# Optimization experiments

Measured on AMD Instinct MI355X. Metric: run time of the kernel, lower is better.

Reference implementation:

```python
import jax, jax.numpy as jnp
import numpy as np

BS, S, D, H = 2, 2048, 1024, 16
DH = D // H  # 64


def setup_inputs() -> dict:
    key = jax.random.key(0)
    k1, k2, k3 = jax.random.split(key, 3)
    x = jax.random.normal(k1, (BS, S, D), dtype=jnp.float32)
    w_qkv = jax.random.normal(k2, (D, H, 3 * DH), dtype=jnp.float32) * (D ** -0.5)
    b_qkv = jnp.zeros((H, 3 * DH), dtype=jnp.float32)
    w_out = jax.random.normal(k3, (H, DH, D), dtype=jnp.float32) * (D ** -0.5)
    b_out = jnp.zeros((D,), dtype=jnp.float32)
    return {"x": x, "w_qkv": w_qkv, "b_qkv": b_qkv, "w_out": w_out, "b_out": b_out}


def reference(x, w_qkv, b_qkv, w_out, b_out):
    dtype = x.dtype
    # QKV projection: DenseGeneral(features=(H, 3*DH)) -> [B, S, H, 3*DH]
    qkv = jnp.einsum("bsd,dhf->bshf", x, w_qkv) + b_qkv
    q, k, v = jnp.split(qkv, 3, axis=-1)  # each [B, S, H, DH]

    scale = DH ** -0.5
    q = (q * scale).astype(jnp.float32)
    k = k.astype(jnp.float32)
    # Full causal attention with fp32 scores (as in original)
    weights = jnp.einsum("bqhd,bkhd->bhqk", q, k)  # [B, H, S, S]
    causal = jnp.tril(jnp.ones((S, S), dtype=bool))[None, None, :, :]
    weights = jnp.where(causal, weights, jnp.finfo(jnp.float32).min)
    weights = jax.nn.softmax(weights, axis=-1).astype(dtype)
    attn = jnp.einsum("bhqk,bkhd->bqhd", weights, v).astype(dtype)

    # Output projection: DenseGeneral(D, axis=(-2, -1))
    out = jnp.einsum("bqhd,hdo->bqo", attn, w_out) + b_out
    return out
```

## Files before the change

kernel.cpp:

```cpp
#include <hip/hip_runtime.h>
#include <hip/hip_bf16.h>
#include <stdint.h>

#define NBS 2
#define SEQ 2048
#define DMODEL 1024
#define NH 16
#define DHEAD 64
#define MROWS (NBS*SEQ)
#define NQKV (NH*3*DHEAD)

typedef __bf16 bf16;
typedef __bf16 bf16x8 __attribute__((ext_vector_type(8)));
typedef float f32x4 __attribute__((ext_vector_type(4)));
typedef float f32x16 __attribute__((ext_vector_type(16)));
typedef unsigned int u32x2 __attribute__((ext_vector_type(2)));

#define LOG2E 1.44269504088896f
#define QSCALE (0.125f * LOG2E)
#define KSTR 72

static __device__ __forceinline__ void gload_lds16(const bf16* g, bf16* l) {
    __builtin_amdgcn_global_load_lds(
        (const __attribute__((address_space(1))) uint32_t*)g,
        (__attribute__((address_space(3))) uint32_t*)l, 16, 0, 0);
}

static __device__ __forceinline__ bf16x8 ld_b8(const bf16* p) {
    return __builtin_bit_cast(bf16x8, *(const uint4*)p);
}

static __device__ __forceinline__ uint32_t pk_bf16(float lo, float hi) {
    unsigned short l = __builtin_bit_cast(unsigned short, (bf16)lo);
    unsigned short h = __builtin_bit_cast(unsigned short, (bf16)hi);
    return ((uint32_t)h << 16) | (uint32_t)l;
}

static __device__ __forceinline__ u32x2 lane_swap32(uint32_t a, uint32_t b, int lane) {
#if __has_builtin(__builtin_amdgcn_permlane32_swap)
    return __builtin_amdgcn_permlane32_swap(a, b, false, false);
#else
    uint32_t sa = __shfl_xor(a, 32), sb = __shfl_xor(b, 32);
    u32x2 r;
    r.x = (lane >= 32) ? sb : a;
    r.y = (lane >= 32) ? b : sa;
    return r;
#endif
}

__global__ __launch_bounds__(256) void k_prep(
        const float* __restrict__ x, const float* __restrict__ w_qkv,
        const float* __restrict__ w_out,
        bf16* __restrict__ xb, bf16* __restrict__ wqkT, bf16* __restrict__ woT) {
    __shared__ float t[32][33];
    int bid = blockIdx.x, tid = threadIdx.x;
    if (bid < 4096) {
        int i = bid * 256 + tid;
        float4 v = ((const float4*)x)[i];
        ushort4 o;
        o.x = __builtin_bit_cast(unsigned short, (bf16)v.x);
        o.y = __builtin_bit_cast(unsigned short, (bf16)v.y);
        o.z = __builtin_bit_cast(unsigned short, (bf16)v.z);
        o.w = __builtin_bit_cast(unsigned short, (bf16)v.w);
        ((ushort4*)xb)[i] = o;
    } else if (bid < 7168) {
        int lb = bid - 4096;
        int bx = lb % 96, by = lb / 96;
        int tx = tid & 31, ty = tid >> 5;
        int r0 = by * 32, c0 = bx * 32;
#pragma unroll
        for (int i = 0; i < 4; i++)
            t[ty + i*8][tx] = w_qkv[(size_t)(r0 + ty + i*8) * NQKV + (c0 + tx)];
        __syncthreads();
#pragma unroll
        for (int i = 0; i < 4; i++) {
            int c = c0 + ty + i*8;
            int h = c / 192, f = c % 192;
            int cperm = ((f >> 6) << 10) + (h << 6) + (f & 63);
            wqkT[(size_t)cperm * DMODEL + (r0 + tx)] = (bf16)t[tx][ty + i*8];
        }
    } else {
        int lb = bid - 7168;
        int bx = lb & 31, by = lb >> 5;
        int tx = tid & 31, ty = tid >> 5;
        int r0 = by * 32, c0 = bx * 32;
#pragma unroll
        for (int i = 0; i < 4; i++)
            t[ty + i*8][tx] = w_out[(size_t)(r0 + ty + i*8) * DMODEL + (c0 + tx)];
        __syncthreads();
#pragma unroll
        for (int i = 0; i < 4; i++)
            woT[(size_t)(c0 + ty + i*8) * DMODEL + (r0 + tx)] = (bf16)t[tx][ty + i*8];
    }
}

#define G1_NT 16

__global__ __launch_bounds__(512, 2) void k_gemm_qkv(
        const bf16* __restrict__ A, const bf16* __restrict__ Bt,
        const float* __restrict__ bias,
        bf16* __restrict__ Q, bf16* __restrict__ Kp, bf16* __restrict__ Vt) {
    __shared__ __align__(16) bf16 As[2][256*64];
    __shared__ __align__(16) bf16 Bs[2][192*64];
    int tid = threadIdx.x;
    int wid = tid >> 6, lane = tid & 63;
    int wr = wid >> 2, wc = wid & 3;
    int g = lane >> 4, r = lane & 15;

    int lid = blockIdx.y * 16 + blockIdx.x;
    int swz = (lid & 7) * 32 + (lid >> 3);
    int tile_n = (swz % 16) * 192, tile_m = (swz / 16) * 256;

    f32x4 acc[8][3];
#pragma unroll
    for (int m = 0; m < 8; m++)
#pragma unroll
        for (int n = 0; n < 3; n++)
            acc[m][n] = (f32x4){0.f, 0.f, 0.f, 0.f};

    int srowA[4], schkA[4], srowB[3], schkB[3];
#pragma unroll
    for (int j2 = 0; j2 < 4; j2++) {
        int idx = tid + j2 * 512;
        srowA[j2] = idx >> 3;
        schkA[j2] = ((idx & 7) ^ (srowA[j2] & 7)) * 8;
    }
#pragma unroll
    for (int j2 = 0; j2 < 3; j2++) {
        int idx = tid + j2 * 512;
        srowB[j2] = idx >> 3;
        schkB[j2] = ((idx & 7) ^ (srowB[j2] & 7)) * 8;
    }

#define G1_STAGE(buf, k0)                                                          \
    {                                                                              \
        _Pragma("unroll")                                                          \
        for (int j2 = 0; j2 < 4; j2++)                                             \
            gload_lds16(A + (size_t)(tile_m + srowA[j2]) * DMODEL + (k0) + schkA[j2], \
                        As[buf] + (tid + j2*512) * 8);                             \
        _Pragma("unroll")                                                          \
        for (int j2 = 0; j2 < 3; j2++)                                             \
            gload_lds16(Bt + (size_t)(tile_n + srowB[j2]) * DMODEL + (k0) + schkB[j2], \
                        Bs[buf] + (tid + j2*512) * 8);                             \
    }

    G1_STAGE(0, 0);

    int r7 = r & 7;
    for (int t = 0; t < G1_NT; t++) {
        int cur = t & 1;
        if (t + 1 < G1_NT) {
            G1_STAGE(cur ^ 1, (t + 1) * 64);
            asm volatile("s_waitcnt vmcnt(7)" ::: "memory");
        } else {
            asm volatile("s_waitcnt vmcnt(0)" ::: "memory");
        }
        __builtin_amdgcn_s_barrier();
        __builtin_amdgcn_sched_barrier(0);

        const bf16* pa = As[cur];
        const bf16* pb = Bs[cur];
#pragma unroll
        for (int kk = 0; kk < 2; kk++) {
            int rchk = ((kk*4 + g) ^ r7) * 8;
            bf16x8 bfr[3];
#pragma unroll
            for (int n = 0; n < 3; n++)
                bfr[n] = ld_b8(pb + (wc*48 + n*16 + r) * 64 + rchk);
#pragma unroll
            for (int m = 0; m < 8; m++) {
                bf16x8 af = ld_b8(pa + (wr*128 + m*16 + r) * 64 + rchk);
#pragma unroll
                for (int n = 0; n < 3; n++)
                    acc[m][n] = __builtin_amdgcn_mfma_f32_16x16x32_bf16(af, bfr[n], acc[m][n], 0, 0, 0);
            }
        }
        asm volatile("s_waitcnt lgkmcnt(0)" ::: "memory");
        __builtin_amdgcn_s_barrier();
    }

#pragma unroll
    for (int m = 0; m < 8; m++) {
#pragma unroll
        for (int n = 0; n < 3; n++) {
            int col = tile_n + wc*48 + n*16 + r;
            int kind = col >> 10;
            int h = (col >> 6) & 15;
            int d = col & 63;
            float bv = bias[h*192 + (kind << 6) + d];
            if (kind == 2) {
                int row0 = tile_m + wr*128 + m*16 + g*4;
                int b = row0 >> 11, s0 = row0 & 2047;
                ushort4 vv;
                vv.x = __builtin_bit_cast(unsigned short, (bf16)(acc[m][n][0] + bv));
                vv.y = __builtin_bit_cast(unsigned short, (bf16)(acc[m][n][1] + bv));
                vv.z = __builtin_bit_cast(unsigned short, (bf16)(acc[m][n][2] + bv));
                vv.w = __builtin_bit_cast(unsigned short, (bf16)(acc[m][n][3] + bv));
                *(ushort4*)&Vt[(((size_t)(b*NH + h)) * DHEAD + d) * SEQ + s0] = vv;
            } else {
#pragma unroll
                for (int j = 0; j < 4; j++) {
                    int row = tile_m + wr*128 + m*16 + g*4 + j;
                    int b = row >> 11, s = row & 2047;
                    float v = acc[m][n][j] + bv;
                    size_t addr = (((size_t)(b*NH + h)) * SEQ + s) * DHEAD + d;
                    if (kind == 0) Q[addr]  = (bf16)(v * QSCALE);
                    else           Kp[addr] = (bf16)v;
                }
            }
        }
    }
#undef G1_STAGE
}

__global__ __launch_bounds__(256) void k_gemm_out(
        const bf16* __restrict__ A, const bf16* __restrict__ Bt,
        const float* __restrict__ bias, float* __restrict__ out) {
    __shared__ __align__(16) bf16 As[2][64*32];
    __shared__ __align__(16) bf16 Bs[2][128*32];
    int tid = threadIdx.x;
    int wave = tid >> 6, lane = tid & 63;
    int g = lane >> 4, r = lane & 15;
    int srow = lane >> 2, schunk = (lane & 3) * 8;
    int tile_m = blockIdx.y * 64, tile_n = blockIdx.x * 128;

    f32x4 acc[4][2];
#pragma unroll
    for (int m = 0; m < 4; m++)
#pragma unroll
        for (int n = 0; n < 2; n++)
            acc[m][n] = (f32x4){0.f, 0.f, 0.f, 0.f};

#define GO_STAGE(buf, k0)                                                                 \
    {                                                                                     \
        gload_lds16(A  + (size_t)(tile_m + wave*16 + srow) * DMODEL + (k0) + schunk,      \
                    As[buf] + wave*512);                                                  \
        gload_lds16(Bt + (size_t)(tile_n + wave*16 + srow) * DMODEL + (k0) + schunk,      \
                    Bs[buf] + wave*512);                                                  \
        gload_lds16(Bt + (size_t)(tile_n + 64 + wave*16 + srow) * DMODEL + (k0) + schunk, \
                    Bs[buf] + 2048 + wave*512);                                           \
    }

    GO_STAGE(0, 0);

    for (int t = 0; t < 32; t++) {
        int cur = t & 1;
        if (t + 1 < 32) {
            GO_STAGE(cur ^ 1, (t + 1) * 32);
            asm volatile("s_waitcnt vmcnt(3)" ::: "memory");
        } else {
            asm volatile("s_waitcnt vmcnt(0)" ::: "memory");
        }
        __builtin_amdgcn_s_barrier();
        __builtin_amdgcn_sched_barrier(0);

        bf16x8 af[4], bfr[2];
#pragma unroll
        for (int m = 0; m < 4; m++) af[m]  = *(const bf16x8*)(As[cur] + (m*16 + r)*32 + g*8);
#pragma unroll
        for (int n = 0; n < 2; n++) bfr[n] = *(const bf16x8*)(Bs[cur] + (wave*32 + n*16 + r)*32 + g*8);
#pragma unroll
        for (int m = 0; m < 4; m++)
#pragma unroll
            for (int n = 0; n < 2; n++)
                acc[m][n] = __builtin_amdgcn_mfma_f32_16x16x32_bf16(af[m], bfr[n], acc[m][n], 0, 0, 0);
        asm volatile("s_waitcnt lgkmcnt(0)" ::: "memory");
        __builtin_amdgcn_s_barrier();
    }
#undef GO_STAGE

#pragma unroll
    for (int m = 0; m < 4; m++) {
#pragma unroll
        for (int n = 0; n < 2; n++) {
            int col = tile_n + wave*32 + n*16 + r;
            float bv = bias[col];
#pragma unroll
            for (int j = 0; j < 4; j++) {
                int row = tile_m + m*16 + g*4 + j;
                out[(size_t)row * DMODEL + col] = acc[m][n][j] + bv;
            }
        }
    }
}

#define QBLK 128
#define KVB 64

static __device__ __forceinline__ void attn_tile_body(
        const bf16* Ks, const bf16* VsT,
        const bf16x8 qa2[4], const bf16x8& ones,
        f32x16 o32[2], f32x16& acc_l,
        int kv0, int qb, int qrow, int l31, int hi, int lane) {
    const f32x16 z16 = {0,0,0,0,0,0,0,0,0,0,0,0,0,0,0,0};
    f32x16 st[2];
    st[0] = z16; st[1] = z16;
    __builtin_amdgcn_s_setprio(1);
#pragma unroll
    for (int c = 0; c < 4; c++) {
        bf16x8 kf0 = ld_b8(Ks + l31*KSTR        + c*16 + hi*8);
        bf16x8 kf1 = ld_b8(Ks + (32 + l31)*KSTR + c*16 + hi*8);
        st[0] = __builtin_amdgcn_mfma_f32_32x32x16_bf16(kf0, qa2[c], st[0], 0, 0, 0);
        st[1] = __builtin_amdgcn_mfma_f32_32x32x16_bf16(kf1, qa2[c], st[1], 0, 0, 0);
    }
    __builtin_amdgcn_s_setprio(0);

    bf16x8 vf[2][4];
#pragma unroll
    for (int dblk = 0; dblk < 2; dblk++)
#pragma unroll
        for (int c = 0; c < 4; c++)
            vf[dblk][c] = ld_b8(VsT + (dblk*32 + l31)*KSTR + c*16 + hi*8);

    bool needm = (kv0 + KVB - 1) > qb;
#pragma unroll
    for (int rb = 0; rb < 2; rb++) {
#pragma unroll
        for (int reg = 0; reg < 16; reg++) {
            float e = __builtin_amdgcn_exp2f(st[rb][reg]);
            if (needm) {
                int kv = kv0 + rb*32 + (reg & 3) + 8*(reg >> 2) + 4*hi;
                if (kv > qrow) e = 0.f;
            }
            st[rb][reg] = e;
        }
    }

    bf16x8 pa[4];
#pragma unroll
    for (int c = 0; c < 4; c++) {
        const f32x16& pp = st[c >> 1];
        const int base = (c & 1) * 8;
        uint32_t a0 = pk_bf16(pp[base+0], pp[base+1]);
        uint32_t a1 = pk_bf16(pp[base+2], pp[base+3]);
        uint32_t b0 = pk_bf16(pp[base+4], pp[base+5]);
        uint32_t b1 = pk_bf16(pp[base+6], pp[base+7]);
        u32x2 s0 = lane_swap32(a0, b0, lane);
        u32x2 s1 = lane_swap32(a1, b1, lane);
        uint4 fr = {s0.x, s1.x, s0.y, s1.y};
        pa[c] = __builtin_bit_cast(bf16x8, fr);
    }

    __builtin_amdgcn_s_setprio(1);
#pragma unroll
    for (int c = 0; c < 4; c++) {
        o32[0] = __builtin_amdgcn_mfma_f32_32x32x16_bf16(pa[c], vf[0][c], o32[0], 0, 0, 0);
        o32[1] = __builtin_amdgcn_mfma_f32_32x32x16_bf16(pa[c], vf[1][c], o32[1], 0, 0, 0);
        acc_l  = __builtin_amdgcn_mfma_f32_32x32x16_bf16(pa[c], ones, acc_l, 0, 0, 0);
    }
    __builtin_amdgcn_s_setprio(0);
}

__device__ const int8_t JQC[32]  = {10,10, 4, 0, 15,15, 3, 1,  9, 9, 7, 2, 13,14, 7, 5,
                                    14,14,11, 5, 15, 8,11, 6,  8,12,12, 6, 13,13,11,12};
__device__ const int8_t JT0[32]  = { 0,11, 0, 0,  0,11, 0, 0,  0,10, 0, 0,  0, 0, 8, 0,
                                    10,20, 0, 6, 22, 0, 8, 0,  9, 0, 9, 7, 10,19,16,18};
__device__ const int8_t JT1[32]  = {11,22,10, 2, 11,22, 8, 4, 10,20, 8, 6, 10,10,16, 6,
                                    20,30, 8,12, 32, 9,16, 7, 18, 9,18,14, 19,28,24,26};
__device__ const int8_t JSEG[32] = { 0, 1, 0, 0,  0, 1, 0, 0,  0, 1, 0, 0,  0, 0, 1, 0,
                                     1, 2, 0, 1,  2, 0, 1, 0,  1, 0, 1, 1,  1, 2, 2, 2};

__global__ __launch_bounds__(256) void k_attn_split(
        const bf16* __restrict__ Q, const bf16* __restrict__ K,
        const bf16* __restrict__ Vt,
        bf16* __restrict__ Op0, bf16* __restrict__ Op1, bf16* __restrict__ Op2,
        float* __restrict__ Lp0, float* __restrict__ Lp1, float* __restrict__ Lp2) {
    int scu = blockIdx.x;
    int bh = scu >> 3, slot = scu & 7;
    int j = slot * 4 + blockIdx.y;
    int qc  = JQC[j];
    int t0  = JT0[j];
    int t1  = JT1[j];
    int seg = JSEG[j];
    int q0 = qc * QBLK;
    int tid = threadIdx.x, wave = tid >> 6, lane = tid & 63;
    int l31 = lane & 31, hi = lane >> 5;

    __shared__ __align__(16) bf16 Ks[2][KVB*KSTR];
    __shared__ __align__(16) bf16 VsT[2][KVB*KSTR];

    const bf16* Kg = K  + (size_t)bh * SEQ * DHEAD;
    const bf16* Vg = Vt + (size_t)bh * DHEAD * SEQ;

    int qb = q0 + wave * 32;
    int qrow = qb + l31;

    const bf16* qrow_p = Q + ((size_t)bh * SEQ + qrow) * DHEAD;
    bf16x8 qa2[4];
#pragma unroll
    for (int c = 0; c < 4; c++) qa2[c] = ld_b8(qrow_p + c*16 + hi*8);

    bf16x8 ones;
#pragma unroll
    for (int c = 0; c < 8; c++) ones[c] = (bf16)1.0f;

    const f32x16 z16 = {0,0,0,0,0,0,0,0,0,0,0,0,0,0,0,0};
    f32x16 o32[2], acc_l;
    o32[0] = z16; o32[1] = z16; acc_l = z16;

    int qmax_wave = qb + 31;

    int srow = tid >> 3, sc8 = (tid & 7) * 8;
    int wK0 = srow*KSTR + sc8;
    int wK1 = (srow+32)*KSTR + sc8;

    bf16x8 kreg[2], vreg[2];
    {
        int kvs = t0 * KVB;
        kreg[0] = ld_b8(Kg + (size_t)(kvs + srow)      * DHEAD + sc8);
        kreg[1] = ld_b8(Kg + (size_t)(kvs + srow + 32) * DHEAD + sc8);
        vreg[0] = ld_b8(Vg + (size_t)srow      * SEQ + kvs + sc8);
        vreg[1] = ld_b8(Vg + (size_t)(srow+32) * SEQ + kvs + sc8);
    }

    int cur = 0;
    for (int t = t0; t < t1; t++) {
        int kv0 = t * KVB;
        *(uint4*)&Ks[cur][wK0]  = __builtin_bit_cast(uint4, kreg[0]);
        *(uint4*)&Ks[cur][wK1]  = __builtin_bit_cast(uint4, kreg[1]);
        *(uint4*)&VsT[cur][wK0] = __builtin_bit_cast(uint4, vreg[0]);
        *(uint4*)&VsT[cur][wK1] = __builtin_bit_cast(uint4, vreg[1]);
        __syncthreads();

        if (t + 1 < t1) {
            int kv1 = kv0 + KVB;
            kreg[0] = ld_b8(Kg + (size_t)(kv1 + srow)      * DHEAD + sc8);
            kreg[1] = ld_b8(Kg + (size_t)(kv1 + srow + 32) * DHEAD + sc8);
            vreg[0] = ld_b8(Vg + (size_t)srow      * SEQ + kv1 + sc8);
            vreg[1] = ld_b8(Vg + (size_t)(srow+32) * SEQ + kv1 + sc8);
        }

        if (kv0 <= qmax_wave)
            attn_tile_body(Ks[cur], VsT[cur], qa2, ones, o32, acc_l,
                           kv0, qb, qrow, l31, hi, lane);
        cur ^= 1;
    }

    bf16* Op; float* Lp; size_t obase; int lbase;
    if (seg == 0)      { Op = Op0; Lp = Lp0; obase = ((size_t)bh*2048 + q0) * 64;          lbase = bh*2048 + q0; }
    else if (seg == 1) { Op = Op1; Lp = Lp1; obase = ((size_t)bh*1408 + (qc-5)*128) * 64;  lbase = bh*1408 + (qc-5)*128; }
    else               { Op = Op2; Lp = Lp2; obase = ((size_t)bh*640  + (qc-11)*128) * 64; lbase = bh*640  + (qc-11)*128; }

    if (l31 == 0) {
#pragma unroll
        for (int reg = 0; reg < 16; reg++) {
            int qr = (reg & 3) + 8*(reg >> 2) + 4*hi;
            Lp[lbase + wave*32 + qr] = acc_l[reg];
        }
    }

#pragma unroll
    for (int reg = 0; reg < 16; reg++) {
        int qr = (reg & 3) + 8*(reg >> 2) + 4*hi;
        size_t base = obase + (size_t)(wave*32 + qr) * 64 + l31;
        Op[base]      = (bf16)o32[0][reg];
        Op[base + 32] = (bf16)o32[1][reg];
    }
}

__global__ __launch_bounds__(256) void k_merge(
        const bf16* __restrict__ Op0, const bf16* __restrict__ Op1,
        const bf16* __restrict__ Op2,
        const float* __restrict__ Lp0, const float* __restrict__ Lp1,
        const float* __restrict__ Lp2,
        bf16* __restrict__ Oa) {
    int g = blockIdx.x * 256 + threadIdx.x;
    int dseg = g & 7;
    int s = (g >> 3) & 2047;
    int bh = g >> 14;
    int qc = s >> 7;
    int sl = s & 127;

    size_t r0 = ((size_t)bh * 2048 + s) * 64 + dseg*8;
    bf16x8 p0 = ld_b8(Op0 + r0);
    float l = Lp0[bh*2048 + s];
    float acc[8];
#pragma unroll
    for (int i = 0; i < 8; i++) acc[i] = (float)p0[i];

    if (qc >= 5) {
        size_t r1 = ((size_t)bh * 1408 + (qc-5)*128 + sl) * 64 + dseg*8;
        bf16x8 p1 = ld_b8(Op1 + r1);
        l += Lp1[bh*1408 + (qc-5)*128 + sl];
#pragma unroll
        for (int i = 0; i < 8; i++) acc[i] += (float)p1[i];
        if (qc >= 11) {
            size_t r2 = ((size_t)bh * 640 + (qc-11)*128 + sl) * 64 + dseg*8;
            bf16x8 p2 = ld_b8(Op2 + r2);
            l += Lp2[bh*640 + (qc-11)*128 + sl];
#pragma unroll
            for (int i = 0; i < 8; i++) acc[i] += (float)p2[i];
        }
    }

    float inv = 1.0f / l;
    bf16x8 r;
#pragma unroll
    for (int i = 0; i < 8; i++) r[i] = (bf16)(acc[i] * inv);
    int b = bh >> 4, h = bh & 15;
    *(uint4*)&Oa[(((size_t)b * SEQ + s) * NH + h) * DHEAD + dseg*8] =
        __builtin_bit_cast(uint4, r);
}

__global__ __launch_bounds__(256) void k_attn(
        const bf16* __restrict__ Q, const bf16* __restrict__ K,
        const bf16* __restrict__ Vt, bf16* __restrict__ O) {
    int bh = blockIdx.y;
    int qc = (bh >= 16) ? (15 - (int)blockIdx.x) : (int)blockIdx.x;
    int q0 = qc * QBLK;
    int tid = threadIdx.x, wave = tid >> 6, lane = tid & 63;
    int l31 = lane & 31, hi = lane >> 5;

    __shared__ __align__(16) bf16 Ks[2][KVB*KSTR];
    __shared__ __align__(16) bf16 VsT[2][KVB*KSTR];

    const bf16* Kg = K  + (size_t)bh * SEQ * DHEAD;
    const bf16* Vg = Vt + (size_t)bh * DHEAD * SEQ;

    int qb = q0 + wave * 32;
    int qrow = qb + l31;

    const bf16* qrow_p = Q + ((size_t)bh * SEQ + qrow) * DHEAD;
    bf16x8 qa2[4];
#pragma unroll
    for (int c = 0; c < 4; c++) qa2[c] = ld_b8(qrow_p + c*16 + hi*8);

    bf16x8 ones;
#pragma unroll
    for (int c = 0; c < 8; c++) ones[c] = (bf16)1.0f;

    const f32x16 z16 = {0,0,0,0,0,0,0,0,0,0,0,0,0,0,0,0};
    f32x16 o32[2], acc_l;
    o32[0] = z16; o32[1] = z16; acc_l = z16;

    int nt = 2*qc + 2;
    int qmax_wave = qb + 31;

    int srow = tid >> 3, sc8 = (tid & 7) * 8;
    int wK0 = srow*KSTR + sc8;
    int wK1 = (srow+32)*KSTR + sc8;

    bf16x8 kreg[2], vreg[2];
    kreg[0] = ld_b8(Kg + (size_t)srow      * DHEAD + sc8);
    kreg[1] = ld_b8(Kg + (size_t)(srow+32) * DHEAD + sc8);
    vreg[0] = ld_b8(Vg + (size_t)srow      * SEQ + sc8);
    vreg[1] = ld_b8(Vg + (size_t)(srow+32) * SEQ + sc8);

    int cur = 0;
    for (int t = 0; t < nt; t++) {
        int kv0 = t * KVB;
        *(uint4*)&Ks[cur][wK0]  = __builtin_bit_cast(uint4, kreg[0]);
        *(uint4*)&Ks[cur][wK1]  = __builtin_bit_cast(uint4, kreg[1]);
        *(uint4*)&VsT[cur][wK0] = __builtin_bit_cast(uint4, vreg[0]);
        *(uint4*)&VsT[cur][wK1] = __builtin_bit_cast(uint4, vreg[1]);
        __syncthreads();

        if (t + 1 < nt) {
            int kv1 = kv0 + KVB;
            kreg[0] = ld_b8(Kg + (size_t)(kv1 + srow)      * DHEAD + sc8);
            kreg[1] = ld_b8(Kg + (size_t)(kv1 + srow + 32) * DHEAD + sc8);
            vreg[0] = ld_b8(Vg + (size_t)srow      * SEQ + kv1 + sc8);
            vreg[1] = ld_b8(Vg + (size_t)(srow+32) * SEQ + kv1 + sc8);
        }

        if (kv0 <= qmax_wave)
            attn_tile_body(Ks[cur], VsT[cur], qa2, ones, o32, acc_l,
                           kv0, qb, qrow, l31, hi, lane);
        cur ^= 1;
    }

    int b = bh >> 4, h = bh & 15;
#pragma unroll
    for (int reg = 0; reg < 16; reg++) {
        int qr = (reg & 3) + 8*(reg >> 2) + 4*hi;
        int srow2 = q0 + wave*32 + qr;
        float linv = 1.0f / acc_l[reg];
        size_t base = (((size_t)b * SEQ + srow2) * NH + h) * DHEAD + l31;
        O[base]      = (bf16)(o32[0][reg] * linv);
        O[base + 32] = (bf16)(o32[1][reg] * linv);
    }
}


extern "C" void kernel_launch(void* const* d_in, const int* in_sizes, int n_in,
                              void* d_out, int out_size, void* d_ws, size_t ws_size,
                              hipStream_t stream) {
    const float* x     = (const float*)d_in[0];
    const float* w_qkv = (const float*)d_in[1];
    const float* b_qkv = (const float*)d_in[2];
    const float* w_out = (const float*)d_in[3];
    const float* b_out = (const float*)d_in[4];
    float* out = (float*)d_out;

    char* ws = (char*)d_ws;
    bf16* xb   = (bf16*)(ws);
    bf16* wqkT = (bf16*)(ws + 8388608);
    bf16* woT  = (bf16*)(ws + 14680064);
    bf16* qb   = (bf16*)(ws + 16777216);
    bf16* kb   = (bf16*)(ws + 25165824);
    bf16* vb   = (bf16*)(ws + 33554432);
    bf16* Op0  = (bf16*)(ws + 41943040);
    bf16* Op1  = (bf16*)(ws + 50331648);
    bf16* Op2  = (bf16*)(ws + 56098816);
    float* Lp0 = (float*)(ws + 8388608);
    float* Lp1 = (float*)(ws + 8388608 + 262144);
    float* Lp2 = (float*)(ws + 8388608 + 524288);
    const size_t WS_NEED = 58720256;
    bf16* attn = xb;

    k_prep<<<8192, 256, 0, stream>>>(x, w_qkv, w_out, xb, wqkT, woT);

    k_gemm_qkv<<<dim3(16, 16), 512, 0, stream>>>(xb, wqkT, b_qkv, qb, kb, vb);

    if (ws_size >= WS_NEED) {
        k_attn_split<<<dim3(256, 4), 256, 0, stream>>>(qb, kb, vb,
                                                       Op0, Op1, Op2, Lp0, Lp1, Lp2);
        k_merge<<<(NBS*NH*SEQ*DHEAD/8)/256, 256, 0, stream>>>(Op0, Op1, Op2,
                                                              Lp0, Lp1, Lp2, attn);
    } else {
        k_attn<<<dim3(SEQ/QBLK, NBS*NH), 256, 0, stream>>>(qb, kb, vb, attn);
    }

    k_gemm_out<<<dim3(DMODEL/128, MROWS/64), 256, 0, stream>>>(attn, woT, b_out, out);
}
```

Measured before the change: 115.3 us.

## Fuse split-attention merge into output projection GEMM A-tile loading

Removes the separate merge kernel and instead combines the three partial attention outputs and their normalizers while loading A tiles in the output GEMM. This drops one kernel launch plus the write and reread of the merged attention tensor. In exchange, each of the 8 column-tile blocks redoes the merge for its rows, and every load reads all three partials unconditionally, masked by multipliers. Those reads use clamped indices, so they fetch real but unused data, adding global traffic to the GEMM's critical path.

```diff
diff --git a/kernel.cpp b/kernel.cpp
--- a/kernel.cpp
+++ b/kernel.cpp
@@ -213,6 +213,117 @@
 #undef G1_STAGE
 }
 
+__global__ __launch_bounds__(256) void k_gemm_out_f(
+        const bf16* __restrict__ Op0, const bf16* __restrict__ Op1,
+        const bf16* __restrict__ Op2,
+        const float* __restrict__ Lp0, const float* __restrict__ Lp1,
+        const float* __restrict__ Lp2,
+        const bf16* __restrict__ Bt, const float* __restrict__ bias,
+        float* __restrict__ out) {
+    __shared__ __align__(16) bf16 As[2][64*32];
+    __shared__ __align__(16) bf16 Bs[2][128*32];
+    int tid = threadIdx.x;
+    int wave = tid >> 6, lane = tid & 63;
+    int g = lane >> 4, r = lane & 15;
+    int srow = lane >> 2, schunk = (lane & 3) * 8;
+    int tile_m = blockIdx.y * 64, tile_n = blockIdx.x * 128;
+
+    int row = tile_m + wave*16 + srow;
+    int b = row >> 11, s = row & 2047;
+    int qc = s >> 7, sl = s & 127;
+    int qc5  = (qc >= 5)  ? qc - 5  : 0;
+    int qc11 = (qc >= 11) ? qc - 11 : 0;
+    float u1 = (qc >= 5)  ? 1.f : 0.f;
+    float u2 = (qc >= 11) ? 1.f : 0.f;
+    int i1 = qc5*128 + sl, i2 = qc11*128 + sl;
+
+    f32x4 acc[4][2];
+#pragma unroll
+    for (int m = 0; m < 4; m++)
+#pragma unroll
+        for (int n = 0; n < 2; n++)
+            acc[m][n] = (f32x4){0.f, 0.f, 0.f, 0.f};
+
+#define A_LOAD(t, p0v, p1v, p2v, l0v, l1v, l2v)                                   \
+    {                                                                             \
+        int h_ = (t) >> 1, d0_ = ((t) & 1) * 32 + schunk;                         \
+        int bh_ = b*16 + h_;                                                      \
+        p0v = *(const uint4*)&Op0[((size_t)bh_*2048 + s)*64 + d0_];               \
+        p1v = *(const uint4*)&Op1[((size_t)bh_*1408 + i1)*64 + d0_];              \
+        p2v = *(const uint4*)&Op2[((size_t)bh_*640  + i2)*64 + d0_];              \
+        l0v = Lp0[bh_*2048 + s]; l1v = Lp1[bh_*1408 + i1]; l2v = Lp2[bh_*640 + i2]; \
+    }
+
+#define A_MERGE(buf, p0v, p1v, p2v, l0v, l1v, l2v)                                \
+    {                                                                             \
+        bf16x8 q0_ = __builtin_bit_cast(bf16x8, p0v);                             \
+        bf16x8 q1_ = __builtin_bit_cast(bf16x8, p1v);                             \
+        bf16x8 q2_ = __builtin_bit_cast(bf16x8, p2v);                             \
+        float inv_ = 1.0f / (l0v + u1*l1v + u2*l2v);                              \
+        bf16x8 mg_;                                                               \
+        _Pragma("unroll")                                                         \
+        for (int i_ = 0; i_ < 8; i_++)                                            \
+            mg_[i_] = (bf16)((((float)q0_[i_]) + u1*(float)q1_[i_]                \
+                              + u2*(float)q2_[i_]) * inv_);                       \
+        *(uint4*)&As[buf][(wave*16 + srow)*32 + schunk] =                         \
+            __builtin_bit_cast(uint4, mg_);                                       \
+    }
+
+#define B_STAGE(buf, k0)                                                                  \
+    {                                                                                     \
+        gload_lds16(Bt + (size_t)(tile_n + wave*16 + srow) * DMODEL + (k0) + schunk,      \
+                    Bs[buf] + wave*512);                                                  \
+        gload_lds16(Bt + (size_t)(tile_n + 64 + wave*16 + srow) * DMODEL + (k0) + schunk, \
+                    Bs[buf] + 2048 + wave*512);                                           \
+    }
+
+    uint4 pa0, pa1, pa2;
+    float la0, la1, la2;
+
+    A_LOAD(0, pa0, pa1, pa2, la0, la1, la2);
+    B_STAGE(0, 0);
+    A_MERGE(0, pa0, pa1, pa2, la0, la1, la2);
+    __syncthreads();
+
+    for (int t = 0; t < 32; t++) {
+        int cur = t & 1;
+        if (t + 1 < 32) {
+            A_LOAD(t + 1, pa0, pa1, pa2, la0, la1, la2);
+            B_STAGE(cur ^ 1, (t + 1) * 32);
+        }
+        bf16x8 af[4], bfr[2];
+#pragma unroll
+        for (int m = 0; m < 4; m++) af[m]  = *(const bf16x8*)(As[cur] + (m*16 + r)*32 + g*8);
+#pragma unroll
+        for (int n = 0; n < 2; n++) bfr[n] = *(const bf16x8*)(Bs[cur] + (wave*32 + n*16 + r)*32 + g*8);
+#pragma unroll
+        for (int m = 0; m < 4; m++)
+#pragma unroll
+            for (int n = 0; n < 2; n++)
+                acc[m][n] = __builtin_amdgcn_mfma_f32_16x16x32_bf16(af[m], bfr[n], acc[m][n], 0, 0, 0);
+        if (t + 1 < 32)
+            A_MERGE(cur ^ 1, pa0, pa1, pa2, la0, la1, la2);
+        __syncthreads();
+    }
+#undef A_LOAD
+#undef A_MERGE
+#undef B_STAGE
+
+#pragma unroll
+    for (int m = 0; m < 4; m++) {
+#pragma unroll
+        for (int n = 0; n < 2; n++) {
+            int col = tile_n + wave*32 + n*16 + r;
+            float bv = bias[col];
+#pragma unroll
+            for (int j = 0; j < 4; j++) {
+                int orow = tile_m + m*16 + g*4 + j;
+                out[(size_t)orow * DMODEL + col] = acc[m][n][j] + bv;
+            }
+        }
+    }
+}
+
 __global__ __launch_bounds__(256) void k_gemm_out(
         const bf16* __restrict__ A, const bf16* __restrict__ Bt,
         const float* __restrict__ bias, float* __restrict__ out) {
@@ -458,50 +569,6 @@
     }
 }
 
-__global__ __launch_bounds__(256) void k_merge(
-        const bf16* __restrict__ Op0, const bf16* __restrict__ Op1,
-        const bf16* __restrict__ Op2,
-        const float* __restrict__ Lp0, const float* __restrict__ Lp1,
-        const float* __restrict__ Lp2,
-        bf16* __restrict__ Oa) {
-    int g = blockIdx.x * 256 + threadIdx.x;
-    int dseg = g & 7;
-    int s = (g >> 3) & 2047;
-    int bh = g >> 14;
-    int qc = s >> 7;
-    int sl = s & 127;
-
-    size_t r0 = ((size_t)bh * 2048 + s) * 64 + dseg*8;
-    bf16x8 p0 = ld_b8(Op0 + r0);
-    float l = Lp0[bh*2048 + s];
-    float acc[8];
-#pragma unroll
-    for (int i = 0; i < 8; i++) acc[i] = (float)p0[i];
-
-    if (qc >= 5) {
-        size_t r1 = ((size_t)bh * 1408 + (qc-5)*128 + sl) * 64 + dseg*8;
-        bf16x8 p1 = ld_b8(Op1 + r1);
-        l += Lp1[bh*1408 + (qc-5)*128 + sl];
-#pragma unroll
-        for (int i = 0; i < 8; i++) acc[i] += (float)p1[i];
-        if (qc >= 11) {
-            size_t r2 = ((size_t)bh * 640 + (qc-11)*128 + sl) * 64 + dseg*8;
-            bf16x8 p2 = ld_b8(Op2 + r2);
-            l += Lp2[bh*640 + (qc-11)*128 + sl];
-#pragma unroll
-            for (int i = 0; i < 8; i++) acc[i] += (float)p2[i];
-        }
-    }
-
-    float inv = 1.0f / l;
-    bf16x8 r;
-#pragma unroll
-    for (int i = 0; i < 8; i++) r[i] = (bf16)(acc[i] * inv);
-    int b = bh >> 4, h = bh & 15;
-    *(uint4*)&Oa[(((size_t)b * SEQ + s) * NH + h) * DHEAD + dseg*8] =
-        __builtin_bit_cast(uint4, r);
-}
-
 __global__ __launch_bounds__(256) void k_attn(
         const bf16* __restrict__ Q, const bf16* __restrict__ K,
         const bf16* __restrict__ Vt, bf16* __restrict__ O) {
@@ -615,11 +682,10 @@
     if (ws_size >= WS_NEED) {
         k_attn_split<<<dim3(256, 4), 256, 0, stream>>>(qb, kb, vb,
                                                        Op0, Op1, Op2, Lp0, Lp1, Lp2);
-        k_merge<<<(NBS*NH*SEQ*DHEAD/8)/256, 256, 0, stream>>>(Op0, Op1, Op2,
-                                                              Lp0, Lp1, Lp2, attn);
+        k_gemm_out_f<<<dim3(DMODEL/128, MROWS/64), 256, 0, stream>>>(
+            Op0, Op1, Op2, Lp0, Lp1, Lp2, woT, b_out, out);
     } else {
         k_attn<<<dim3(SEQ/QBLK, NBS*NH), 256, 0, stream>>>(qb, kb, vb, attn);
-    }
-
-    k_gemm_out<<<dim3(DMODEL/128, MROWS/64), 256, 0, stream>>>(attn, woT, b_out, out);
-}
+        k_gemm_out<<<dim3(DMODEL/128, MROWS/64), 256, 0, stream>>>(attn, woT, b_out, out);
+    }
+}
```

Result: slower. 122.3 us (+6.1%).
